# Optimization experiments

Measured on AMD Instinct MI355X. Metric: run time of the kernel, lower is better.

## Reference

```python
import jax, jax.numpy as jnp
import numpy as np

B, S = 2, 256
CN, CE = 256, 128        # node / edge channels
A, H, V = 32, 8, 32      # attention_size, heads, value_size
AH, VH = A * H, V * H


def setup_inputs() -> dict:
    key = jax.random.key(0)
    ks = jax.random.split(key, 16)
    w = lambda k, shape: (jax.random.normal(k, shape) * 0.05).astype(jnp.float32)
    nodes = jax.random.normal(ks[0], (B, CN, S), dtype=jnp.float32)
    edges = jax.random.normal(ks[1], (B, CE, S, S), dtype=jnp.float32)
    lengths = jnp.array([S, (3 * S) // 4])            # padded-batch valid lengths
    mask = jnp.arange(S)[None, :] < lengths[:, None]  # (B, S) bool
    return dict(
        nodes=nodes, edges=edges, mask=mask,
        Wq=w(ks[2], (AH, CN)),
        Wk=w(ks[3], (AH, CN + CE)),
        Wv=w(ks[4], (VH, CN + CE)),
        Wo=w(ks[5], (CN, VH)),
        We=w(ks[6], (CE, VH + CE)),
        Wm1=w(ks[7], (CN, CN)), bm1=jnp.zeros((CN,), jnp.float32),
        Wm2=w(ks[8], (CN, CN)), bm2=jnp.zeros((CN,), jnp.float32),
        We1=w(ks[9], (CE, CE)), be1=jnp.zeros((CE,), jnp.float32),
        We2=w(ks[10], (CE, CE)), be2=jnp.zeros((CE,), jnp.float32),
        an0=(jax.random.normal(ks[11], (CN,)) * 0.1).astype(jnp.float32),
        an1=(jax.random.normal(ks[12], (CN,)) * 0.1).astype(jnp.float32),
        ae0=(jax.random.normal(ks[13], (CE,)) * 0.1).astype(jnp.float32),
        ae1=(jax.random.normal(ks[14], (CE,)) * 0.1).astype(jnp.float32),
    )


def _block(nodes, edges, mask, Wq, Wk, Wv, Wo, We,
           Wm1, bm1, Wm2, bm2, We1, be1, We2, be2, an0, an1, ae0, ae1):
    relu = jax.nn.relu
    b, _, s = nodes.shape
    # node MLP (1x1 conv, ReLU, 1x1 conv, ReLU) + ReZero residual; dropout in eval mode = identity
    h = relu(jnp.einsum('oc,bcs->bos', Wm1, nodes) + bm1[None, :, None])
    h = relu(jnp.einsum('oc,bcs->bos', Wm2, h) + bm2[None, :, None])
    nodes = nodes + an0[None, :, None] * h
    # edge MLP (1x1 conv2d) + ReZero residual
    g = relu(jnp.einsum('oc,bcij->boij', We1, edges) + be1[None, :, None, None])
    g = relu(jnp.einsum('oc,bcij->boij', We2, g) + be2[None, :, None, None])
    edges = edges + ae0[None, :, None, None] * g
    # materialized multi-head attention
    q = jnp.einsum('ac,bcs->bas', Wq, nodes).reshape(b, H, A, s)            # (B,H,A,S)
    ne = jnp.concatenate([jnp.broadcast_to(nodes[:, :, :, None], (b, CN, s, s)), edges], axis=1)
    k = jnp.einsum('ac,bcij->baij', Wk, ne).reshape(b, H, A, s, s)          # (B,H,A,S,S)
    v = jnp.einsum('vc,bcij->bvij', Wv, ne).reshape(b, H, V, s, s)          # (B,H,V,S,S)
    sim = jnp.einsum('bhai,bhaij->bhij', q, k) / jnp.sqrt(jnp.float32(A))   # (B,H,S,S)
    sim = jnp.where(mask[:, None, None, :], sim, jnp.float32(-1e9))
    sim = jax.nn.softmax(sim, axis=-1)
    mm = (mask[:, None, None, :] & mask[:, None, :, None]).astype(sim.dtype)  # (B,1,S,S)
    sim = sim * mm
    v = v * mm[:, None]
    nf = jnp.einsum('bhij,bhvij->bhvi', sim, v).reshape(b, H * V, s)        # (B,HV,S)
    node_att = jnp.einsum('oc,bcs->bos', Wo, nf)
    # edge features: broadcast node features along j, symmetrize via transpose+average
    ef = 0.5 * (nf[:, :, :, None] + nf[:, :, None, :])                      # (B,HV,S,S)
    edge_att = jnp.einsum('oc,bcij->boij', We, jnp.concatenate([ef, edges], axis=1))
    # ReZero residuals (project_* are Identity since in_size == out_size)
    nodes = nodes + an1[None, :, None] * node_att
    edges = edges + ae1[None, :, None, None] * edge_att
    # final masking
    nodes = nodes * mask[:, None, :].astype(nodes.dtype)
    edges = edges * mm
    return nodes, edges


def reference(nodes, edges, mask, Wq, Wk, Wv, Wo, We, Wm1, bm1, Wm2, bm2,
              We1, be1, We2, be2, an0, an1, ae0, ae1):
    return _block(nodes, edges, mask, Wq, Wk, Wv, Wo, We,
                  Wm1, bm1, Wm2, bm2, We1, be1, We2, be2, an0, an1, ae0, ae1)
```

## Files before the change

### kernel.cpp

```cpp
#include <hip/hip_runtime.h>
#include <hip/hip_bf16.h>
#include <cstdint>
#include <cstddef>

constexpr int B_  = 2;
constexpr int S_  = 256;
constexpr int CN_ = 256;
constexpr int CE_ = 128;
constexpr int A_  = 32;
constexpr int H_  = 8;
constexpr int V_  = 32;
constexpr int AH_ = A_ * H_;
constexpr int VH_ = V_ * H_;
constexpr int SS_ = S_ * S_;
constexpr int CNE_ = CN_ + CE_;

constexpr size_t OFF_N1   = 0;
constexpr size_t OFF_Q    = OFF_N1  + (size_t)B_*CN_*S_;
constexpr size_t OFF_VN   = OFF_Q   + (size_t)B_*AH_*S_;
constexpr size_t OFF_NF   = OFF_VN  + (size_t)B_*VH_*S_;
constexpr size_t OFF_WNF  = OFF_NF  + (size_t)B_*VH_*S_;
constexpr size_t OFF_SE   = OFF_WNF + (size_t)B_*CE_*S_;
constexpr size_t OFF_WB1  = OFF_SE  + (size_t)B_*S_*1024;
constexpr size_t OFF_WB2  = OFF_WB1 + 16384;
constexpr size_t OFF_WBE  = OFF_WB2 + 16384;
constexpr size_t OFF_MASK = OFF_WBE + 16384;

__device__ inline uint16_t f2bf(float x) {
    uint32_t u = __float_as_uint(x);
    uint32_t r = (u + 0x7fffu + ((u >> 16) & 1u)) >> 16;
    return (uint16_t)r;
}
__device__ inline float bf2f(uint16_t h) {
    return __uint_as_float(((uint32_t)h) << 16);
}

typedef __attribute__((ext_vector_type(8))) short sh8;
typedef __attribute__((ext_vector_type(4))) short sh4;
typedef __attribute__((ext_vector_type(4))) float f32x4;

#define MFMA_B16(a, b, c) __builtin_amdgcn_mfma_f32_16x16x32_bf16((a), (b), (c), 0, 0, 0)

__device__ inline int eidx(int j, int c) {
    return (j * 136 + c) ^ (((j >> 3) & 7) << 3);
}

__global__ void k_mask_norm(const unsigned char* __restrict__ mraw,
                            float* __restrict__ ws)
{
    int t = threadIdx.x;
    unsigned char b1 = mraw[1], b2 = mraw[2];
    float mv;
    if (b1 == (unsigned char)1) {
        mv = mraw[t] ? 1.f : 0.f;
    } else if (b2 == (unsigned char)128) {
        mv = (((const float*)mraw)[t] != 0.f) ? 1.f : 0.f;
    } else {
        mv = (((const int*)mraw)[t] != 0) ? 1.f : 0.f;
    }
    ws[OFF_MASK + t] = mv;
}

__global__ void k_wprep(const float* __restrict__ We1_,
                        const float* __restrict__ We2_,
                        const float* __restrict__ We_,
                        float* __restrict__ ws)
{
    int idx = blockIdx.x * 256 + threadIdx.x;
    int m = idx >> 14;
    int r = idx & 16383;
    int o = r >> 7, c = r & 127;
    ushort* wb1 = (ushort*)(ws + OFF_WB1);
    ushort* wb2 = (ushort*)(ws + OFF_WB2);
    ushort* wbe = (ushort*)(ws + OFF_WBE);
    if (m == 0)      wb1[r] = f2bf(We1_[o*CE_ + c]);
    else if (m == 1) wb2[r] = f2bf(We2_[o*CE_ + c]);
    else             wbe[r] = f2bf(We_[o*CNE_ + CN_ + c]);
}

__global__ __launch_bounds__(256)
void k_node_mlp_qv(const float* __restrict__ nodes,
                   const float* __restrict__ Wm1, const float* __restrict__ bm1,
                   const float* __restrict__ Wm2, const float* __restrict__ bm2,
                   const float* __restrict__ an0,
                   const float* __restrict__ Wq,  const float* __restrict__ Wv,
                   float* __restrict__ ws)
{
    __shared__ float xs[CN_ * 8];
    __shared__ float hs[CN_ * 8];
    const int t  = threadIdx.x;
    const int b  = blockIdx.x >> 5;
    const int s0 = (blockIdx.x & 31) * 8;

    #pragma unroll
    for (int r = 0; r < 8; ++r) {
        int idx = r*256 + t;
        int c = idx >> 3, s = idx & 7;
        xs[c*8+s] = nodes[((size_t)(b*CN_+c))*S_ + s0 + s];
    }
    __syncthreads();

    float acc[8];
    {
        float bv = bm1[t];
        #pragma unroll
        for (int s = 0; s < 8; ++s) acc[s] = bv;
        for (int c = 0; c < CN_; ++c) {
            float w = Wm1[t*CN_ + c];
            #pragma unroll
            for (int s = 0; s < 8; ++s) acc[s] = fmaf(w, xs[c*8+s], acc[s]);
        }
        #pragma unroll
        for (int s = 0; s < 8; ++s) hs[t*8+s] = fmaxf(acc[s], 0.f);
    }
    __syncthreads();
    {
        float bv = bm2[t];
        #pragma unroll
        for (int s = 0; s < 8; ++s) acc[s] = bv;
        for (int c = 0; c < CN_; ++c) {
            float w = Wm2[t*CN_ + c];
            #pragma unroll
            for (int s = 0; s < 8; ++s) acc[s] = fmaf(w, hs[c*8+s], acc[s]);
        }
    }
    float a0 = an0[t];
    #pragma unroll
    for (int s = 0; s < 8; ++s) {
        float n1 = xs[t*8+s] + a0 * fmaxf(acc[s], 0.f);
        xs[t*8+s] = n1;
        ws[OFF_N1 + ((size_t)(b*CN_+t))*S_ + s0 + s] = n1;
    }
    __syncthreads();

    {
        #pragma unroll
        for (int s = 0; s < 8; ++s) acc[s] = 0.f;
        for (int c = 0; c < CN_; ++c) {
            float w = Wq[t*CN_ + c];
            #pragma unroll
            for (int s = 0; s < 8; ++s) acc[s] = fmaf(w, xs[c*8+s], acc[s]);
        }
        const float rsA = 0.1767766952966369f;
        #pragma unroll
        for (int s = 0; s < 8; ++s)
            ws[OFF_Q + ((size_t)(b*AH_+t))*S_ + s0 + s] = acc[s] * rsA;
    }
    {
        #pragma unroll
        for (int s = 0; s < 8; ++s) acc[s] = 0.f;
        for (int c = 0; c < CN_; ++c) {
            float w = Wv[t*CNE_ + c];
            #pragma unroll
            for (int s = 0; s < 8; ++s) acc[s] = fmaf(w, xs[c*8+s], acc[s]);
        }
        #pragma unroll
        for (int s = 0; s < 8; ++s)
            ws[OFF_VN + ((size_t)(b*VH_+t))*S_ + s0 + s] = acc[s];
    }
}

__global__ __launch_bounds__(256, 2)
void k_edge_mlp(const float* __restrict__ edges,
                const float* __restrict__ ws,
                const float* __restrict__ be1, const float* __restrict__ be2,
                const float* __restrict__ ae0,
                float* __restrict__ e1out)
{
    __shared__ ushort Ehi[64 * 136];
    __shared__ ushort Elo[64 * 136];
    __shared__ ushort Ht [64 * 136];

    const int t  = threadIdx.x;
    const int b  = blockIdx.x >> 10;
    const int i  = (blockIdx.x >> 2) & 255;
    const int j0 = (blockIdx.x & 3) * 64;
    const float* Eb = edges + (size_t)b*CE_*SS_ + (size_t)i*S_ + j0;

    {
        const int tj = t & 15;
        const int p0 = t >> 4;
        #pragma unroll
        for (int s = 0; s < 4; ++s) {
            int c = (s*16 + p0) * 2;
            float4 v0 = *(const float4*)(Eb + (size_t)c*SS_ + tj*4);
            float4 v1 = *(const float4*)(Eb + (size_t)(c+1)*SS_ + tj*4);
            float a0[4] = {v0.x, v0.y, v0.z, v0.w};
            float a1[4] = {v1.x, v1.y, v1.z, v1.w};
            #pragma unroll
            for (int jj = 0; jj < 4; ++jj) {
                int j = tj*4 + jj;
                uint16_t h0 = f2bf(a0[jj]); uint16_t l0 = f2bf(a0[jj] - bf2f(h0));
                uint16_t h1 = f2bf(a1[jj]); uint16_t l1 = f2bf(a1[jj] - bf2f(h1));
                int us = eidx(j, c);
                *(uint32_t*)&Ehi[us] = (uint32_t)h0 | ((uint32_t)h1 << 16);
                *(uint32_t*)&Elo[us] = (uint32_t)l0 | ((uint32_t)l1 << 16);
            }
        }
    }

    const int w  = t >> 6;
    const int l  = t & 63;
    const int lr = l & 15;
    const int lk = l >> 4;
    const ushort* wb1 = (const ushort*)(ws + OFF_WB1);
    const ushort* wb2 = (const ushort*)(ws + OFF_WB2);
    sh8 A1[2][4], A2[2][4];
    #pragma unroll
    for (int mt = 0; mt < 2; ++mt) {
        int o = w*32 + mt*16 + lr;
        #pragma unroll
        for (int ks = 0; ks < 4; ++ks) {
            A1[mt][ks] = *(const sh8*)(wb1 + o*CE_ + ks*32 + lk*8);
            A2[mt][ks] = *(const sh8*)(wb2 + o*CE_ + ks*32 + lk*8);
        }
    }

    f32x4 acc1[2][4];
    #pragma unroll
    for (int mt = 0; mt < 2; ++mt) {
        float4 bv = *(const float4*)(be1 + w*32 + mt*16 + lk*4);
        #pragma unroll
        for (int nt = 0; nt < 4; ++nt) {
            acc1[mt][nt][0] = bv.x; acc1[mt][nt][1] = bv.y;
            acc1[mt][nt][2] = bv.z; acc1[mt][nt][3] = bv.w;
        }
    }
    __syncthreads();
    #pragma unroll
    for (int nt = 0; nt < 4; ++nt) {
        int j = nt*16 + lr;
        sh8 bh[4], bl[4];
        #pragma unroll
        for (int ks = 0; ks < 4; ++ks) {
            int us = eidx(j, ks*32 + lk*8);
            bh[ks] = *(const sh8*)&Ehi[us];
            bl[ks] = *(const sh8*)&Elo[us];
        }
        #pragma unroll
        for (int mt = 0; mt < 2; ++mt)
            #pragma unroll
            for (int ks = 0; ks < 4; ++ks) {
                acc1[mt][nt] = MFMA_B16(A1[mt][ks], bh[ks], acc1[mt][nt]);
                acc1[mt][nt] = MFMA_B16(A1[mt][ks], bl[ks], acc1[mt][nt]);
            }
    }

    #pragma unroll
    for (int mt = 0; mt < 2; ++mt)
        #pragma unroll
        for (int nt = 0; nt < 4; ++nt) {
            int o0 = w*32 + mt*16 + lk*4;
            int j  = nt*16 + lr;
            float h0 = fmaxf(acc1[mt][nt][0], 0.f);
            float h1 = fmaxf(acc1[mt][nt][1], 0.f);
            float h2 = fmaxf(acc1[mt][nt][2], 0.f);
            float h3 = fmaxf(acc1[mt][nt][3], 0.f);
            int us = eidx(j, o0);
            *(uint32_t*)&Ht[us]     = (uint32_t)f2bf(h0) | ((uint32_t)f2bf(h1) << 16);
            *(uint32_t*)&Ht[us + 2] = (uint32_t)f2bf(h2) | ((uint32_t)f2bf(h3) << 16);
        }
    __syncthreads();

    f32x4 acc2[2][4];
    #pragma unroll
    for (int mt = 0; mt < 2; ++mt) {
        float4 bv = *(const float4*)(be2 + w*32 + mt*16 + lk*4);
        #pragma unroll
        for (int nt = 0; nt < 4; ++nt) {
            acc2[mt][nt][0] = bv.x; acc2[mt][nt][1] = bv.y;
            acc2[mt][nt][2] = bv.z; acc2[mt][nt][3] = bv.w;
        }
    }
    #pragma unroll
    for (int nt = 0; nt < 4; ++nt) {
        int j = nt*16 + lr;
        sh8 hh[4];
        #pragma unroll
        for (int ks = 0; ks < 4; ++ks)
            hh[ks] = *(const sh8*)&Ht[eidx(j, ks*32 + lk*8)];
        #pragma unroll
        for (int mt = 0; mt < 2; ++mt)
            #pragma unroll
            for (int ks = 0; ks < 4; ++ks)
                acc2[mt][nt] = MFMA_B16(A2[mt][ks], hh[ks], acc2[mt][nt]);
    }

    #pragma unroll
    for (int mt = 0; mt < 2; ++mt) {
        int o0 = w*32 + mt*16 + lk*4;
        float4 a0v = *(const float4*)(ae0 + o0);
        float aev[4] = {a0v.x, a0v.y, a0v.z, a0v.w};
        #pragma unroll
        for (int nt = 0; nt < 4; ++nt) {
            int j = nt*16 + lr;
            int us = eidx(j, o0);
            sh4 eh = *(const sh4*)&Ehi[us];
            sh4 el = *(const sh4*)&Elo[us];
            #pragma unroll
            for (int r = 0; r < 4; ++r) {
                float e = bf2f((uint16_t)eh[r]) + bf2f((uint16_t)el[r]);
                float g = fmaxf(acc2[mt][nt][r], 0.f);
                e1out[(size_t)(b*CE_ + o0 + r)*SS_ + (size_t)i*S_ + j0 + j] = e + aev[r]*g;
            }
        }
    }
}

__global__ __launch_bounds__(256)
void k_attn(const float* __restrict__ e1, float* __restrict__ ws,
            const float* __restrict__ Wk)
{
    __shared__ float qcol[AH_];
    __shared__ float qw[CE_ * 8];
    __shared__ float simL[H_ * S_];
    __shared__ float Etile[CE_ * 65];
    const int t = threadIdx.x;
    const int b = blockIdx.x >> 8, i = blockIdx.x & 255;
    const float* maskf = ws + OFF_MASK;

    qcol[t] = ws[OFF_Q + ((size_t)(b*AH_+t))*S_ + i];
    __syncthreads();
    #pragma unroll
    for (int k = 0; k < 4; ++k) {
        int idx = k*256 + t;
        int c = idx >> 3, h = idx & 7;
        float a = 0.f;
        #pragma unroll
        for (int aa = 0; aa < A_; ++aa)
            a = fmaf(qcol[h*A_ + aa], Wk[(h*A_+aa)*CNE_ + CN_ + c], a);
        qw[c*8 + h] = a;
    }
    __syncthreads();

    const float* Eb = e1 + ((size_t)(b*CE_)*S_ + i)*S_;
    float sv[8];
    #pragma unroll
    for (int h = 0; h < 8; ++h) sv[h] = 0.f;
    for (int c = 0; c < CE_; ++c) {
        float e = Eb[(size_t)c*SS_ + t];
        float4 q0 = *(const float4*)(qw + c*8);
        float4 q1 = *(const float4*)(qw + c*8 + 4);
        sv[0] = fmaf(q0.x, e, sv[0]); sv[1] = fmaf(q0.y, e, sv[1]);
        sv[2] = fmaf(q0.z, e, sv[2]); sv[3] = fmaf(q0.w, e, sv[3]);
        sv[4] = fmaf(q1.x, e, sv[4]); sv[5] = fmaf(q1.y, e, sv[5]);
        sv[6] = fmaf(q1.z, e, sv[6]); sv[7] = fmaf(q1.w, e, sv[7]);
    }
    const bool mj = maskf[b*S_ + t] != 0.f;
    #pragma unroll
    for (int h = 0; h < 8; ++h) simL[h*S_ + t] = mj ? sv[h] : -1e9f;
    __syncthreads();

    {
        const int h = t >> 5, l = t & 31;
        float vv[8]; float m = -3.4e38f;
        #pragma unroll
        for (int k = 0; k < 8; ++k) { vv[k] = simL[h*S_ + l + k*32]; m = fmaxf(m, vv[k]); }
        #pragma unroll
        for (int off = 16; off >= 1; off >>= 1) m = fmaxf(m, __shfl_xor(m, off, 32));
        float ssum = 0.f; float ex[8];
        #pragma unroll
        for (int k = 0; k < 8; ++k) { ex[k] = __expf(vv[k] - m); ssum += ex[k]; }
        #pragma unroll
        for (int off = 16; off >= 1; off >>= 1) ssum += __shfl_xor(ssum, off, 32);
        const float mi = maskf[b*S_ + i];
        const float rr = mi / ssum;
        #pragma unroll
        for (int k = 0; k < 8; ++k) simL[h*S_ + l + k*32] = ex[k] * rr;
    }
    __syncthreads();

    const int cp = t & 127, hg = t >> 7;
    float a4[4] = {0.f, 0.f, 0.f, 0.f};
    for (int jt = 0; jt < 4; ++jt) {
        #pragma unroll 4
        for (int r = 0; r < 32; ++r) {
            int idx = r*256 + t;
            int c = idx >> 6, j = idx & 63;
            Etile[c*65 + j] = Eb[(size_t)c*SS_ + jt*64 + j];
        }
        __syncthreads();
        for (int j = 0; j < 64; ++j) {
            float e = Etile[cp*65 + j];
            #pragma unroll
            for (int k = 0; k < 4; ++k)
                a4[k] = fmaf(e, simL[(hg*4+k)*S_ + jt*64 + j], a4[k]);
        }
        __syncthreads();
    }
    float* se = ws + OFF_SE + (size_t)(b*S_ + i)*1024;
    #pragma unroll
    for (int k = 0; k < 4; ++k) se[(hg*4+k)*128 + cp] = a4[k];
}

__global__ __launch_bounds__(256)
void k_nf(float* __restrict__ ws, const float* __restrict__ Wv)
{
    __shared__ float seL[1024];
    const int t = threadIdx.x;
    const int b = blockIdx.x >> 8, i = blockIdx.x & 255;
    const float* se = ws + OFF_SE + (size_t)(b*S_ + i)*1024;
    #pragma unroll
    for (int k = 0; k < 4; ++k) seL[k*256 + t] = se[k*256 + t];
    __syncthreads();
    const int h = t >> 5;
    float acc = 0.f;
    for (int c = 0; c < CE_; ++c)
        acc = fmaf(Wv[t*CNE_ + CN_ + c], seL[h*128 + c], acc);
    const float mi = ws[OFF_MASK + b*S_ + i];
    float nfv = ws[OFF_VN + ((size_t)(b*VH_+t))*S_ + i] * mi + acc;
    ws[OFF_NF + ((size_t)(b*VH_+t))*S_ + i] = nfv;
}

__global__ __launch_bounds__(256)
void k_node_out(float* __restrict__ ws, const float* __restrict__ Wo,
                const float* __restrict__ We, const float* __restrict__ an1,
                float* __restrict__ out_nodes)
{
    __shared__ float xs[VH_ * 8];
    const int t  = threadIdx.x;
    const int b  = blockIdx.x >> 5;
    const int s0 = (blockIdx.x & 31) * 8;
    #pragma unroll
    for (int r = 0; r < 8; ++r) {
        int idx = r*256 + t; int c = idx >> 3, s = idx & 7;
        xs[c*8+s] = ws[OFF_NF + ((size_t)(b*VH_+c))*S_ + s0 + s];
    }
    __syncthreads();
    float acc[8] = {0,0,0,0,0,0,0,0};
    for (int c = 0; c < VH_; ++c) {
        float w = Wo[t*VH_ + c];
        #pragma unroll
        for (int s = 0; s < 8; ++s) acc[s] = fmaf(w, xs[c*8+s], acc[s]);
    }
    float a1 = an1[t];
    #pragma unroll
    for (int s = 0; s < 8; ++s) {
        float mi = ws[OFF_MASK + b*S_ + s0 + s];
        out_nodes[((size_t)(b*CN_+t))*S_ + s0 + s] =
            (ws[OFF_N1 + ((size_t)(b*CN_+t))*S_ + s0 + s] + a1*acc[s]) * mi;
    }
    if (t < CE_) {
        float acc2[8] = {0,0,0,0,0,0,0,0};
        for (int c = 0; c < VH_; ++c) {
            float w = We[t*CNE_ + c];
            #pragma unroll
            for (int s = 0; s < 8; ++s) acc2[s] = fmaf(w, xs[c*8+s], acc2[s]);
        }
        #pragma unroll
        for (int s = 0; s < 8; ++s)
            ws[OFF_WNF + ((size_t)(b*CE_+t))*S_ + s0 + s] = acc2[s];
    }
}

__global__ __launch_bounds__(256, 2)
void k_edge_out(float* __restrict__ e1, const float* __restrict__ ws,
                const float* __restrict__ ae1)
{
    __shared__ ushort Ehi[64 * 136];
    __shared__ ushort Elo[64 * 136];
    __shared__ float  wni_s[CE_];

    const int t  = threadIdx.x;
    const int b  = blockIdx.x >> 10;
    const int i  = (blockIdx.x >> 2) & 255;
    const int j0 = (blockIdx.x & 3) * 64;
    float* Eb = e1 + (size_t)b*CE_*SS_ + (size_t)i*S_ + j0;
    const float* Wnf   = ws + OFF_WNF;
    const float* maskf = ws + OFF_MASK;

    if (t < CE_) wni_s[t] = Wnf[(size_t)(b*CE_ + t)*S_ + i];

    {
        const int tj = t & 15;
        const int p0 = t >> 4;
        #pragma unroll
        for (int s = 0; s < 4; ++s) {
            int c = (s*16 + p0) * 2;
            float4 v0 = *(const float4*)(Eb + (size_t)c*SS_ + tj*4);
            float4 v1 = *(const float4*)(Eb + (size_t)(c+1)*SS_ + tj*4);
            float a0[4] = {v0.x, v0.y, v0.z, v0.w};
            float a1[4] = {v1.x, v1.y, v1.z, v1.w};
            #pragma unroll
            for (int jj = 0; jj < 4; ++jj) {
                int j = tj*4 + jj;
                uint16_t h0 = f2bf(a0[jj]); uint16_t l0 = f2bf(a0[jj] - bf2f(h0));
                uint16_t h1 = f2bf(a1[jj]); uint16_t l1 = f2bf(a1[jj] - bf2f(h1));
                int us = eidx(j, c);
                *(uint32_t*)&Ehi[us] = (uint32_t)h0 | ((uint32_t)h1 << 16);
                *(uint32_t*)&Elo[us] = (uint32_t)l0 | ((uint32_t)l1 << 16);
            }
        }
    }

    const int w  = t >> 6;
    const int l  = t & 63;
    const int lr = l & 15;
    const int lk = l >> 4;
    const ushort* wbe = (const ushort*)(ws + OFF_WBE);
    sh8 AE[2][4];
    #pragma unroll
    for (int mt = 0; mt < 2; ++mt) {
        int o = w*32 + mt*16 + lr;
        #pragma unroll
        for (int ks = 0; ks < 4; ++ks)
            AE[mt][ks] = *(const sh8*)(wbe + o*CE_ + ks*32 + lk*8);
    }

    f32x4 acc[2][4];
    #pragma unroll
    for (int mt = 0; mt < 2; ++mt)
        #pragma unroll
        for (int nt = 0; nt < 4; ++nt)
            acc[mt][nt] = (f32x4){0.f, 0.f, 0.f, 0.f};
    __syncthreads();
    #pragma unroll
    for (int nt = 0; nt < 4; ++nt) {
        int j = nt*16 + lr;
        sh8 bh[4], bl[4];
        #pragma unroll
        for (int ks = 0; ks < 4; ++ks) {
            int us = eidx(j, ks*32 + lk*8);
            bh[ks] = *(const sh8*)&Ehi[us];
            bl[ks] = *(const sh8*)&Elo[us];
        }
        #pragma unroll
        for (int mt = 0; mt < 2; ++mt)
            #pragma unroll
            for (int ks = 0; ks < 4; ++ks) {
                acc[mt][nt] = MFMA_B16(AE[mt][ks], bh[ks], acc[mt][nt]);
                acc[mt][nt] = MFMA_B16(AE[mt][ks], bl[ks], acc[mt][nt]);
            }
    }

    const float mi = maskf[b*S_ + i];
    #pragma unroll
    for (int mt = 0; mt < 2; ++mt) {
        int o0 = w*32 + mt*16 + lk*4;
        float4 a1v = *(const float4*)(ae1 + o0);
        float aev[4] = {a1v.x, a1v.y, a1v.z, a1v.w};
        #pragma unroll
        for (int nt = 0; nt < 4; ++nt) {
            int j  = nt*16 + lr;
            int jg = j0 + j;
            float mj = maskf[b*S_ + jg];
            int us = eidx(j, o0);
            sh4 eh = *(const sh4*)&Ehi[us];
            sh4 el = *(const sh4*)&Elo[us];
            #pragma unroll
            for (int r = 0; r < 4; ++r) {
                float e   = bf2f((uint16_t)eh[r]) + bf2f((uint16_t)el[r]);
                float att = 0.5f*(wni_s[o0+r] + Wnf[(size_t)(b*CE_+o0+r)*S_ + jg])
                          + acc[mt][nt][r];
                Eb[(size_t)(o0+r)*SS_ + j] = (e + aev[r]*att) * (mi * mj);
            }
        }
    }
}

extern "C" void kernel_launch(void* const* d_in, const int* in_sizes, int n_in,
                              void* d_out, int out_size, void* d_ws, size_t ws_size,
                              hipStream_t stream)
{
    const float* nodes = (const float*)d_in[0];
    const float* edges = (const float*)d_in[1];
    const unsigned char* mraw = (const unsigned char*)d_in[2];
    const float* Wq  = (const float*)d_in[3];
    const float* Wk  = (const float*)d_in[4];
    const float* Wv  = (const float*)d_in[5];
    const float* Wo  = (const float*)d_in[6];
    const float* We  = (const float*)d_in[7];
    const float* Wm1 = (const float*)d_in[8];
    const float* bm1 = (const float*)d_in[9];
    const float* Wm2 = (const float*)d_in[10];
    const float* bm2 = (const float*)d_in[11];
    const float* We1 = (const float*)d_in[12];
    const float* be1 = (const float*)d_in[13];
    const float* We2 = (const float*)d_in[14];
    const float* be2 = (const float*)d_in[15];
    const float* an0 = (const float*)d_in[16];
    const float* an1 = (const float*)d_in[17];
    const float* ae0 = (const float*)d_in[18];
    const float* ae1 = (const float*)d_in[19];

    float* ws = (float*)d_ws;
    float* out_nodes = (float*)d_out;
    float* out_edges = out_nodes + (size_t)B_*CN_*S_;

    k_mask_norm  <<<1,    512, 0, stream>>>(mraw, ws);
    k_wprep      <<<192,  256, 0, stream>>>(We1, We2, We, ws);
    k_node_mlp_qv<<<64,   256, 0, stream>>>(nodes, Wm1, bm1, Wm2, bm2, an0, Wq, Wv, ws);
    k_edge_mlp   <<<2048, 256, 0, stream>>>(edges, ws, be1, be2, ae0, out_edges);
    k_attn       <<<512,  256, 0, stream>>>(out_edges, ws, Wk);
    k_nf         <<<512,  256, 0, stream>>>(ws, Wv);
    k_node_out   <<<64,   256, 0, stream>>>(ws, Wo, We, an1, out_nodes);
    k_edge_out   <<<2048, 256, 0, stream>>>(out_edges, ws, ae1);
}
```

Measured before the change: 329.6 us.

## Store edges as packed bf16 hi/lo split, restructure node GEMMs, split qw kernel

The intermediate edge tensor is now stored as a packed hi/lo bf16 pair in one 32-bit word. k_edge_out can then unpack it with bit operations instead of redoing the split rounding, and k_attn unpacks it on load. The hi/lo split now truncates instead of rounding to nearest. The node MLP and node-out kernels change to 4-column tiles with float4 weight loads across twice as many blocks. The per-row q·Wk projection moves out of k_attn into its own k_qw kernel. The changes aim to cut conversion ALU work and raise parallelism in the small GEMMs, at the cost of one extra launch and a slightly different rounding of the stored edges.

```diff
diff --git a/kernel.cpp b/kernel.cpp
--- a/kernel.cpp
+++ b/kernel.cpp
@@ -21,7 +21,8 @@
 constexpr size_t OFF_NF   = OFF_VN  + (size_t)B_*VH_*S_;
 constexpr size_t OFF_WNF  = OFF_NF  + (size_t)B_*VH_*S_;
 constexpr size_t OFF_SE   = OFF_WNF + (size_t)B_*CE_*S_;
-constexpr size_t OFF_WB1  = OFF_SE  + (size_t)B_*S_*1024;
+constexpr size_t OFF_QW   = OFF_SE  + (size_t)B_*S_*1024;
+constexpr size_t OFF_WB1  = OFF_QW  + (size_t)B_*S_*1024;
 constexpr size_t OFF_WB2  = OFF_WB1 + 16384;
 constexpr size_t OFF_WBE  = OFF_WB2 + 16384;
 constexpr size_t OFF_MASK = OFF_WBE + 16384;
@@ -34,6 +35,14 @@
 __device__ inline float bf2f(uint16_t h) {
     return __uint_as_float(((uint32_t)h) << 16);
 }
+__device__ inline uint32_t pack_split(float v) {
+    uint32_t u  = __float_as_uint(v);
+    uint32_t hm = u & 0xffff0000u;
+    return hm | (__float_as_uint(v - __uint_as_float(hm)) >> 16);
+}
+__device__ inline float unpack_f32(uint32_t p) {
+    return __uint_as_float(p & 0xffff0000u) + __uint_as_float(p << 16);
+}
 
 typedef __attribute__((ext_vector_type(8))) short sh8;
 typedef __attribute__((ext_vector_type(4))) short sh4;
@@ -44,6 +53,19 @@
 __device__ inline int eidx(int j, int c) {
     return (j * 136 + c) ^ (((j >> 3) & 7) << 3);
 }
+
+#define GEMM4_K256(WROW, XS, A0, A1, A2, A3)                                   \
+    for (int c = 0; c < 256; c += 4) {                                         \
+        float4 w  = *(const float4*)((WROW) + c);                              \
+        float4 x0 = *(const float4*)((XS) + (c+0)*4);                          \
+        float4 x1 = *(const float4*)((XS) + (c+1)*4);                          \
+        float4 x2 = *(const float4*)((XS) + (c+2)*4);                          \
+        float4 x3 = *(const float4*)((XS) + (c+3)*4);                          \
+        A0 = fmaf(w.x,x0.x,fmaf(w.y,x1.x,fmaf(w.z,x2.x,fmaf(w.w,x3.x,A0))));   \
+        A1 = fmaf(w.x,x0.y,fmaf(w.y,x1.y,fmaf(w.z,x2.y,fmaf(w.w,x3.y,A1))));   \
+        A2 = fmaf(w.x,x0.z,fmaf(w.y,x1.z,fmaf(w.z,x2.z,fmaf(w.w,x3.z,A2))));   \
+        A3 = fmaf(w.x,x0.w,fmaf(w.y,x1.w,fmaf(w.z,x2.w,fmaf(w.w,x3.w,A3))));   \
+    }
 
 __global__ void k_mask_norm(const unsigned char* __restrict__ mraw,
                             float* __restrict__ ws)
@@ -86,78 +108,76 @@
                    const float* __restrict__ Wq,  const float* __restrict__ Wv,
                    float* __restrict__ ws)
 {
-    __shared__ float xs[CN_ * 8];
-    __shared__ float hs[CN_ * 8];
+    __shared__ float xs[CN_ * 4];
+    __shared__ float hs[CN_ * 4];
     const int t  = threadIdx.x;
-    const int b  = blockIdx.x >> 5;
-    const int s0 = (blockIdx.x & 31) * 8;
-
-    #pragma unroll
-    for (int r = 0; r < 8; ++r) {
-        int idx = r*256 + t;
-        int c = idx >> 3, s = idx & 7;
-        xs[c*8+s] = nodes[((size_t)(b*CN_+c))*S_ + s0 + s];
-    }
-    __syncthreads();
-
-    float acc[8];
-    {
-        float bv = bm1[t];
-        #pragma unroll
-        for (int s = 0; s < 8; ++s) acc[s] = bv;
-        for (int c = 0; c < CN_; ++c) {
-            float w = Wm1[t*CN_ + c];
-            #pragma unroll
-            for (int s = 0; s < 8; ++s) acc[s] = fmaf(w, xs[c*8+s], acc[s]);
-        }
-        #pragma unroll
-        for (int s = 0; s < 8; ++s) hs[t*8+s] = fmaxf(acc[s], 0.f);
-    }
-    __syncthreads();
-    {
-        float bv = bm2[t];
-        #pragma unroll
-        for (int s = 0; s < 8; ++s) acc[s] = bv;
-        for (int c = 0; c < CN_; ++c) {
-            float w = Wm2[t*CN_ + c];
-            #pragma unroll
-            for (int s = 0; s < 8; ++s) acc[s] = fmaf(w, hs[c*8+s], acc[s]);
-        }
-    }
-    float a0 = an0[t];
-    #pragma unroll
-    for (int s = 0; s < 8; ++s) {
-        float n1 = xs[t*8+s] + a0 * fmaxf(acc[s], 0.f);
-        xs[t*8+s] = n1;
-        ws[OFF_N1 + ((size_t)(b*CN_+t))*S_ + s0 + s] = n1;
-    }
-    __syncthreads();
-
-    {
-        #pragma unroll
-        for (int s = 0; s < 8; ++s) acc[s] = 0.f;
-        for (int c = 0; c < CN_; ++c) {
-            float w = Wq[t*CN_ + c];
-            #pragma unroll
-            for (int s = 0; s < 8; ++s) acc[s] = fmaf(w, xs[c*8+s], acc[s]);
-        }
+    const int b  = blockIdx.x >> 6;
+    const int s0 = (blockIdx.x & 63) * 4;
+
+    {
+        float4 nv = *(const float4*)(nodes + (size_t)(b*CN_+t)*S_ + s0);
+        xs[t*4+0]=nv.x; xs[t*4+1]=nv.y; xs[t*4+2]=nv.z; xs[t*4+3]=nv.w;
+    }
+    __syncthreads();
+
+    float a0, a1, a2, a3;
+    {
+        float bv = bm1[t]; a0=bv; a1=bv; a2=bv; a3=bv;
+        GEMM4_K256(Wm1 + t*CN_, xs, a0, a1, a2, a3);
+        hs[t*4+0]=fmaxf(a0,0.f); hs[t*4+1]=fmaxf(a1,0.f);
+        hs[t*4+2]=fmaxf(a2,0.f); hs[t*4+3]=fmaxf(a3,0.f);
+    }
+    __syncthreads();
+    {
+        float bv = bm2[t]; a0=bv; a1=bv; a2=bv; a3=bv;
+        GEMM4_K256(Wm2 + t*CN_, hs, a0, a1, a2, a3);
+    }
+    {
+        float an = an0[t];
+        float n0 = xs[t*4+0] + an*fmaxf(a0,0.f);
+        float n1 = xs[t*4+1] + an*fmaxf(a1,0.f);
+        float n2 = xs[t*4+2] + an*fmaxf(a2,0.f);
+        float n3 = xs[t*4+3] + an*fmaxf(a3,0.f);
+        xs[t*4+0]=n0; xs[t*4+1]=n1; xs[t*4+2]=n2; xs[t*4+3]=n3;
+        *(float4*)(ws + OFF_N1 + (size_t)(b*CN_+t)*S_ + s0) = make_float4(n0,n1,n2,n3);
+    }
+    __syncthreads();
+
+    {
+        a0=0.f; a1=0.f; a2=0.f; a3=0.f;
+        GEMM4_K256(Wq + t*CN_, xs, a0, a1, a2, a3);
         const float rsA = 0.1767766952966369f;
-        #pragma unroll
-        for (int s = 0; s < 8; ++s)
-            ws[OFF_Q + ((size_t)(b*AH_+t))*S_ + s0 + s] = acc[s] * rsA;
-    }
-    {
-        #pragma unroll
-        for (int s = 0; s < 8; ++s) acc[s] = 0.f;
-        for (int c = 0; c < CN_; ++c) {
-            float w = Wv[t*CNE_ + c];
-            #pragma unroll
-            for (int s = 0; s < 8; ++s) acc[s] = fmaf(w, xs[c*8+s], acc[s]);
-        }
-        #pragma unroll
-        for (int s = 0; s < 8; ++s)
-            ws[OFF_VN + ((size_t)(b*VH_+t))*S_ + s0 + s] = acc[s];
-    }
+        *(float4*)(ws + OFF_Q + (size_t)(b*AH_+t)*S_ + s0) =
+            make_float4(a0*rsA, a1*rsA, a2*rsA, a3*rsA);
+    }
+    {
+        a0=0.f; a1=0.f; a2=0.f; a3=0.f;
+        GEMM4_K256(Wv + t*CNE_, xs, a0, a1, a2, a3);
+        *(float4*)(ws + OFF_VN + (size_t)(b*VH_+t)*S_ + s0) = make_float4(a0,a1,a2,a3);
+    }
+}
+
+__global__ __launch_bounds__(256)
+void k_qw(float* __restrict__ ws, const float* __restrict__ Wk)
+{
+    __shared__ float qcol[AH_];
+    const int t = threadIdx.x;
+    const int b = blockIdx.x >> 8, i = blockIdx.x & 255;
+    qcol[t] = ws[OFF_Q + (size_t)(b*AH_+t)*S_ + i];
+    __syncthreads();
+    const int c  = t & 127;
+    const int h0 = (t >> 7) * 4;
+    float acc[4] = {0.f, 0.f, 0.f, 0.f};
+    for (int aa = 0; aa < A_; ++aa) {
+        #pragma unroll
+        for (int k = 0; k < 4; ++k) {
+            int ha = (h0 + k)*A_ + aa;
+            acc[k] = fmaf(qcol[ha], Wk[(size_t)ha*CNE_ + CN_ + c], acc[k]);
+        }
+    }
+    float* q = ws + OFF_QW + (size_t)(b*S_ + i)*1024;
+    #pragma unroll
+    for (int k = 0; k < 4; ++k) q[c*8 + h0 + k] = acc[k];
 }
 
 __global__ __launch_bounds__(256, 2)
@@ -165,7 +185,7 @@
                 const float* __restrict__ ws,
                 const float* __restrict__ be1, const float* __restrict__ be2,
                 const float* __restrict__ ae0,
-                float* __restrict__ e1out)
+                uint32_t* __restrict__ e1out)
 {
     __shared__ ushort Ehi[64 * 136];
     __shared__ ushort Elo[64 * 136];
@@ -185,16 +205,19 @@
             int c = (s*16 + p0) * 2;
             float4 v0 = *(const float4*)(Eb + (size_t)c*SS_ + tj*4);
             float4 v1 = *(const float4*)(Eb + (size_t)(c+1)*SS_ + tj*4);
-            float a0[4] = {v0.x, v0.y, v0.z, v0.w};
-            float a1[4] = {v1.x, v1.y, v1.z, v1.w};
+            float q0[4] = {v0.x, v0.y, v0.z, v0.w};
+            float q1[4] = {v1.x, v1.y, v1.z, v1.w};
             #pragma unroll
             for (int jj = 0; jj < 4; ++jj) {
                 int j = tj*4 + jj;
-                uint16_t h0 = f2bf(a0[jj]); uint16_t l0 = f2bf(a0[jj] - bf2f(h0));
-                uint16_t h1 = f2bf(a1[jj]); uint16_t l1 = f2bf(a1[jj] - bf2f(h1));
+                uint32_t u0 = __float_as_uint(q0[jj]), u1 = __float_as_uint(q1[jj]);
+                uint32_t h0m = u0 & 0xffff0000u, h1m = u1 & 0xffff0000u;
+                uint32_t hiw = (u0 >> 16) | h1m;
+                uint32_t low = (__float_as_uint(q0[jj] - __uint_as_float(h0m)) >> 16)
+                             | (__float_as_uint(q1[jj] - __uint_as_float(h1m)) & 0xffff0000u);
                 int us = eidx(j, c);
-                *(uint32_t*)&Ehi[us] = (uint32_t)h0 | ((uint32_t)h1 << 16);
-                *(uint32_t*)&Elo[us] = (uint32_t)l0 | ((uint32_t)l1 << 16);
+                *(uint32_t*)&Ehi[us] = hiw;
+                *(uint32_t*)&Elo[us] = low;
             }
         }
     }
@@ -252,13 +275,13 @@
         for (int nt = 0; nt < 4; ++nt) {
             int o0 = w*32 + mt*16 + lk*4;
             int j  = nt*16 + lr;
-            float h0 = fmaxf(acc1[mt][nt][0], 0.f);
-            float h1 = fmaxf(acc1[mt][nt][1], 0.f);
-            float h2 = fmaxf(acc1[mt][nt][2], 0.f);
-            float h3 = fmaxf(acc1[mt][nt][3], 0.f);
+            uint32_t u0 = __float_as_uint(fmaxf(acc1[mt][nt][0], 0.f));
+            uint32_t u1 = __float_as_uint(fmaxf(acc1[mt][nt][1], 0.f));
+            uint32_t u2 = __float_as_uint(fmaxf(acc1[mt][nt][2], 0.f));
+            uint32_t u3 = __float_as_uint(fmaxf(acc1[mt][nt][3], 0.f));
             int us = eidx(j, o0);
-            *(uint32_t*)&Ht[us]     = (uint32_t)f2bf(h0) | ((uint32_t)f2bf(h1) << 16);
-            *(uint32_t*)&Ht[us + 2] = (uint32_t)f2bf(h2) | ((uint32_t)f2bf(h3) << 16);
+            *(uint32_t*)&Ht[us]     = (u0 >> 16) | (u1 & 0xffff0000u);
+            *(uint32_t*)&Ht[us + 2] = (u2 >> 16) | (u3 & 0xffff0000u);
         }
     __syncthreads();
 
@@ -301,17 +324,16 @@
             for (int r = 0; r < 4; ++r) {
                 float e = bf2f((uint16_t)eh[r]) + bf2f((uint16_t)el[r]);
                 float g = fmaxf(acc2[mt][nt][r], 0.f);
-                e1out[(size_t)(b*CE_ + o0 + r)*SS_ + (size_t)i*S_ + j0 + j] = e + aev[r]*g;
+                e1out[(size_t)(b*CE_ + o0 + r)*SS_ + (size_t)i*S_ + j0 + j] =
+                    pack_split(e + aev[r]*g);
             }
         }
     }
 }
 
 __global__ __launch_bounds__(256)
-void k_attn(const float* __restrict__ e1, float* __restrict__ ws,
-            const float* __restrict__ Wk)
-{
-    __shared__ float qcol[AH_];
+void k_attn(const uint32_t* __restrict__ e1, float* __restrict__ ws)
+{
     __shared__ float qw[CE_ * 8];
     __shared__ float simL[H_ * S_];
     __shared__ float Etile[CE_ * 65];
@@ -319,26 +341,18 @@
     const int b = blockIdx.x >> 8, i = blockIdx.x & 255;
     const float* maskf = ws + OFF_MASK;
 
-    qcol[t] = ws[OFF_Q + ((size_t)(b*AH_+t))*S_ + i];
-    __syncthreads();
-    #pragma unroll
-    for (int k = 0; k < 4; ++k) {
-        int idx = k*256 + t;
-        int c = idx >> 3, h = idx & 7;
-        float a = 0.f;
-        #pragma unroll
-        for (int aa = 0; aa < A_; ++aa)
-            a = fmaf(qcol[h*A_ + aa], Wk[(h*A_+aa)*CNE_ + CN_ + c], a);
-        qw[c*8 + h] = a;
-    }
-    __syncthreads();
-
-    const float* Eb = e1 + ((size_t)(b*CE_)*S_ + i)*S_;
+    {
+        const float4* qwg = (const float4*)(ws + OFF_QW + (size_t)(b*S_ + i)*1024);
+        ((float4*)qw)[t] = qwg[t];
+    }
+    __syncthreads();
+
+    const uint32_t* Eb = e1 + ((size_t)(b*CE_)*S_ + i)*S_;
     float sv[8];
     #pragma unroll
     for (int h = 0; h < 8; ++h) sv[h] = 0.f;
     for (int c = 0; c < CE_; ++c) {
-        float e = Eb[(size_t)c*SS_ + t];
+        float e = unpack_f32(Eb[(size_t)c*SS_ + t]);
         float4 q0 = *(const float4*)(qw + c*8);
         float4 q1 = *(const float4*)(qw + c*8 + 4);
         sv[0] = fmaf(q0.x, e, sv[0]); sv[1] = fmaf(q0.y, e, sv[1]);
@@ -377,7 +391,7 @@
         for (int r = 0; r < 32; ++r) {
             int idx = r*256 + t;
             int c = idx >> 6, j = idx & 63;
-            Etile[c*65 + j] = Eb[(size_t)c*SS_ + jt*64 + j];
+            Etile[c*65 + j] = unpack_f32(Eb[(size_t)c*SS_ + jt*64 + j]);
         }
         __syncthreads();
         for (int j = 0; j < 64; ++j) {
@@ -417,45 +431,35 @@
                 const float* __restrict__ We, const float* __restrict__ an1,
                 float* __restrict__ out_nodes)
 {
-    __shared__ float xs[VH_ * 8];
+    __shared__ float xs[VH_ * 4];
     const int t  = threadIdx.x;
-    const int b  = blockIdx.x >> 5;
-    const int s0 = (blockIdx.x & 31) * 8;
-    #pragma unroll
-    for (int r = 0; r < 8; ++r) {
-        int idx = r*256 + t; int c = idx >> 3, s = idx & 7;
-        xs[c*8+s] = ws[OFF_NF + ((size_t)(b*VH_+c))*S_ + s0 + s];
-    }
-    __syncthreads();
-    float acc[8] = {0,0,0,0,0,0,0,0};
-    for (int c = 0; c < VH_; ++c) {
-        float w = Wo[t*VH_ + c];
-        #pragma unroll
-        for (int s = 0; s < 8; ++s) acc[s] = fmaf(w, xs[c*8+s], acc[s]);
-    }
-    float a1 = an1[t];
-    #pragma unroll
-    for (int s = 0; s < 8; ++s) {
-        float mi = ws[OFF_MASK + b*S_ + s0 + s];
-        out_nodes[((size_t)(b*CN_+t))*S_ + s0 + s] =
-            (ws[OFF_N1 + ((size_t)(b*CN_+t))*S_ + s0 + s] + a1*acc[s]) * mi;
+    const int b  = blockIdx.x >> 6;
+    const int s0 = (blockIdx.x & 63) * 4;
+    {
+        float4 nv = *(const float4*)(ws + OFF_NF + (size_t)(b*VH_+t)*S_ + s0);
+        xs[t*4+0]=nv.x; xs[t*4+1]=nv.y; xs[t*4+2]=nv.z; xs[t*4+3]=nv.w;
+    }
+    __syncthreads();
+    float a0=0.f, a1=0.f, a2=0.f, a3=0.f;
+    GEMM4_K256(Wo + t*VH_, xs, a0, a1, a2, a3);
+    {
+        float aw = an1[t];
+        float4 n1 = *(const float4*)(ws + OFF_N1 + (size_t)(b*CN_+t)*S_ + s0);
+        float4 mk = *(const float4*)(ws + OFF_MASK + b*S_ + s0);
+        *(float4*)(out_nodes + (size_t)(b*CN_+t)*S_ + s0) = make_float4(
+            (n1.x + aw*a0) * mk.x, (n1.y + aw*a1) * mk.y,
+            (n1.z + aw*a2) * mk.z, (n1.w + aw*a3) * mk.w);
     }
     if (t < CE_) {
-        float acc2[8] = {0,0,0,0,0,0,0,0};
-        for (int c = 0; c < VH_; ++c) {
-            float w = We[t*CNE_ + c];
-            #pragma unroll
-            for (int s = 0; s < 8; ++s) acc2[s] = fmaf(w, xs[c*8+s], acc2[s]);
-        }
-        #pragma unroll
-        for (int s = 0; s < 8; ++s)
-            ws[OFF_WNF + ((size_t)(b*CE_+t))*S_ + s0 + s] = acc2[s];
+        a0=0.f; a1=0.f; a2=0.f; a3=0.f;
+        GEMM4_K256(We + t*CNE_, xs, a0, a1, a2, a3);
+        *(float4*)(ws + OFF_WNF + (size_t)(b*CE_+t)*S_ + s0) = make_float4(a0,a1,a2,a3);
     }
 }
 
 __global__ __launch_bounds__(256, 2)
-void k_edge_out(float* __restrict__ e1, const float* __restrict__ ws,
-                const float* __restrict__ ae1)
+void k_edge_out(const uint32_t* __restrict__ e1p, float* __restrict__ e1f,
+                const float* __restrict__ ws, const float* __restrict__ ae1)
 {
     __shared__ ushort Ehi[64 * 136];
     __shared__ ushort Elo[64 * 136];
@@ -465,7 +469,8 @@
     const int b  = blockIdx.x >> 10;
     const int i  = (blockIdx.x >> 2) & 255;
     const int j0 = (blockIdx.x & 3) * 64;
-    float* Eb = e1 + (size_t)b*CE_*SS_ + (size_t)i*S_ + j0;
+    const uint32_t* Ebp = e1p + (size_t)b*CE_*SS_ + (size_t)i*S_ + j0;
+    float*          Ebf = e1f + (size_t)b*CE_*SS_ + (size_t)i*S_ + j0;
     const float* Wnf   = ws + OFF_WNF;
     const float* maskf = ws + OFF_MASK;
 
@@ -477,18 +482,16 @@
         #pragma unroll
         for (int s = 0; s < 4; ++s) {
             int c = (s*16 + p0) * 2;
-            float4 v0 = *(const float4*)(Eb + (size_t)c*SS_ + tj*4);
-            float4 v1 = *(const float4*)(Eb + (size_t)(c+1)*SS_ + tj*4);
-            float a0[4] = {v0.x, v0.y, v0.z, v0.w};
-            float a1[4] = {v1.x, v1.y, v1.z, v1.w};
+            uint4 v0 = *(const uint4*)(Ebp + (size_t)c*SS_ + tj*4);
+            uint4 v1 = *(const uint4*)(Ebp + (size_t)(c+1)*SS_ + tj*4);
+            uint32_t w0[4] = {v0.x, v0.y, v0.z, v0.w};
+            uint32_t w1[4] = {v1.x, v1.y, v1.z, v1.w};
             #pragma unroll
             for (int jj = 0; jj < 4; ++jj) {
                 int j = tj*4 + jj;
-                uint16_t h0 = f2bf(a0[jj]); uint16_t l0 = f2bf(a0[jj] - bf2f(h0));
-                uint16_t h1 = f2bf(a1[jj]); uint16_t l1 = f2bf(a1[jj] - bf2f(h1));
                 int us = eidx(j, c);
-                *(uint32_t*)&Ehi[us] = (uint32_t)h0 | ((uint32_t)h1 << 16);
-                *(uint32_t*)&Elo[us] = (uint32_t)l0 | ((uint32_t)l1 << 16);
+                *(uint32_t*)&Ehi[us] = (w0[jj] >> 16) | (w1[jj] & 0xffff0000u);
+                *(uint32_t*)&Elo[us] = (w0[jj] & 0xffffu) | (w1[jj] << 16);
             }
         }
     }
@@ -552,7 +555,7 @@
                 float e   = bf2f((uint16_t)eh[r]) + bf2f((uint16_t)el[r]);
                 float att = 0.5f*(wni_s[o0+r] + Wnf[(size_t)(b*CE_+o0+r)*S_ + jg])
                           + acc[mt][nt][r];
-                Eb[(size_t)(o0+r)*SS_ + j] = (e + aev[r]*att) * (mi * mj);
+                Ebf[(size_t)(o0+r)*SS_ + j] = (e + aev[r]*att) * (mi * mj);
             }
         }
     }
@@ -589,10 +592,11 @@
 
     k_mask_norm  <<<1,    512, 0, stream>>>(mraw, ws);
     k_wprep      <<<192,  256, 0, stream>>>(We1, We2, We, ws);
-    k_node_mlp_qv<<<64,   256, 0, stream>>>(nodes, Wm1, bm1, Wm2, bm2, an0, Wq, Wv, ws);
-    k_edge_mlp   <<<2048, 256, 0, stream>>>(edges, ws, be1, be2, ae0, out_edges);
-    k_attn       <<<512,  256, 0, stream>>>(out_edges, ws, Wk);
+    k_node_mlp_qv<<<128,  256, 0, stream>>>(nodes, Wm1, bm1, Wm2, bm2, an0, Wq, Wv, ws);
+    k_qw         <<<512,  256, 0, stream>>>(ws, Wk);
+    k_edge_mlp   <<<2048, 256, 0, stream>>>(edges, ws, be1, be2, ae0, (uint32_t*)out_edges);
+    k_attn       <<<512,  256, 0, stream>>>((const uint32_t*)out_edges, ws);
     k_nf         <<<512,  256, 0, stream>>>(ws, Wv);
-    k_node_out   <<<64,   256, 0, stream>>>(ws, Wo, We, an1, out_nodes);
-    k_edge_out   <<<2048, 256, 0, stream>>>(out_edges, ws, ae1);
-}
+    k_node_out   <<<128,  256, 0, stream>>>(ws, Wo, We, an1, out_nodes);
+    k_edge_out   <<<2048, 256, 0, stream>>>((const uint32_t*)out_edges, out_edges, ws, ae1);
+}
```

After: 312.7 us. 1.05x faster.
